# Performance work log

Hardware: AMD Instinct MI355X
Metric: run time of the kernel (lower is better)

## Reference

```python
import jax, jax.numpy as jnp
import numpy as np
import math

INPUT_SIZE = 768
OUTPUT_SIZE = 3072
INS = (8, 12, 8)     # inputs for size=768 (input_size < output_size, no swap)
OUTS = (16, 12, 16)  # outputs
# num singular values via quadratic formula from the torch code
_a = INS[2] * OUTS[2]
_b = INS[0] * OUTS[0] + INS[1] * OUTS[1]
_c = -INPUT_SIZE * OUTPUT_SIZE
NUM_S = int(((-_b + math.sqrt(_b * _b - 4 * _a * _c)) / (2 * _a)) // 1)  # = 134
N_TOKENS = 32768


def _xavier(key, shape, gain):
    # xavier_uniform over first-two-dims fan (matches torch fan computation:
    # fan_in = shape[1]*prod(shape[2:]), fan_out = shape[0]*prod(shape[2:]))
    recf = np.prod(shape[2:]).astype(np.float64) if len(shape) > 2 else 1.0
    fan_in = shape[1] * recf
    fan_out = shape[0] * recf
    bound = gain * math.sqrt(6.0 / (fan_in + fan_out))
    return jax.random.uniform(key, shape, jnp.float32, -bound, bound)


def setup_inputs() -> dict:
    key = jax.random.key(0)
    k0, k1, k2, k3 = jax.random.split(key, 4)
    g = math.sqrt(2.0)
    x = jax.random.normal(k0, (N_TOKENS, INPUT_SIZE), jnp.float32)
    W_1 = _xavier(k1, (INS[0], OUTS[0], NUM_S), g)            # (8,16,134)
    W_2 = _xavier(k2, (NUM_S, INS[1], OUTS[1], NUM_S), g)      # (134,12,12,134)
    W_3 = _xavier(k3, (NUM_S, INS[2], OUTS[2]), g)             # (134,8,16)
    b = jnp.zeros((OUTPUT_SIZE,), jnp.float32)
    return {"x": x, "W_1": W_1, "W_2": W_2, "W_3": W_3, "b": b}


def reference(x, W_1, W_2, W_3, b):
    # W[i,I,a, o,O,bb] = sum_{s,S} W_1[i,o,s] W_2[s,I,O,S] W_3[S,a,bb]
    W = jnp.einsum('ios,sIOS,Sab->iIaoOb', W_1, W_2, W_3)
    # rearrange '(i I a)(o O b)' -> row-major reshape
    W = W.reshape(INPUT_SIZE, OUTPUT_SIZE)
    return x @ W + b
```

## Files before the change

kernel.cpp:

```cpp
#include <hip/hip_runtime.h>


typedef unsigned short u16;
typedef unsigned int   u32;
typedef short s16x8 __attribute__((ext_vector_type(8)));
typedef float f32x4 __attribute__((ext_vector_type(4)));

__device__ __forceinline__ u16 f2bf(float f) {
  u32 u = __float_as_uint(f);
  u32 r = (u + 0x7FFFu + ((u >> 16) & 1u)) >> 16;
  return (u16)r;
}

__device__ __forceinline__ void gload_lds16(const void* g, void* l) {
  __builtin_amdgcn_global_load_lds(
      (const __attribute__((address_space(1))) void*)g,
      (__attribute__((address_space(3))) void*)l, 16, 0, 0);
}

__global__ __launch_bounds__(256) void xconv_kernel(const float* __restrict__ x,
                                                    u16* __restrict__ xb) {
  size_t idx = ((size_t)blockIdx.x * 256 + threadIdx.x) * 8;
  float4 v0 = *(const float4*)(x + idx);
  float4 v1 = *(const float4*)(x + idx + 4);
  uint4 o;
  o.x = (u32)f2bf(v0.x) | ((u32)f2bf(v0.y) << 16);
  o.y = (u32)f2bf(v0.z) | ((u32)f2bf(v0.w) << 16);
  o.z = (u32)f2bf(v1.x) | ((u32)f2bf(v1.y) << 16);
  o.w = (u32)f2bf(v1.z) | ((u32)f2bf(v1.w) << 16);
  *(uint4*)(xb + idx) = o;
}

__global__ __launch_bounds__(256) void a1_kernel(const float* __restrict__ W1,
                                                 const float* __restrict__ W2,
                                                 float* __restrict__ T1) {
  __shared__ float lW1[32 * 136];
  const int t = threadIdx.x;
  const int iog = blockIdx.y;
  const int ios = blockIdx.x * 256 + t;
  for (int idx = t; idx < 32 * 136; idx += 256) {
    int u = idx / 136, s = idx - u * 136;
    lW1[idx] = (s < 134) ? W1[(size_t)(iog * 32 + u) * 134 + s] : 0.f;
  }
  __syncthreads();
  const bool valid = ios < 19296;
  float acc[32];
#pragma unroll
  for (int u = 0; u < 32; u++) acc[u] = 0.f;
  for (int s4 = 0; s4 < 136; s4 += 4) {
    float wa = (valid && s4 + 0 < 134) ? W2[(size_t)(s4 + 0) * 19296 + ios] : 0.f;
    float wb = (valid && s4 + 1 < 134) ? W2[(size_t)(s4 + 1) * 19296 + ios] : 0.f;
    float wc = (valid && s4 + 2 < 134) ? W2[(size_t)(s4 + 2) * 19296 + ios] : 0.f;
    float wd = (valid && s4 + 3 < 134) ? W2[(size_t)(s4 + 3) * 19296 + ios] : 0.f;
#pragma unroll
    for (int u = 0; u < 32; u++) {
      float4 wv = *(const float4*)&lW1[u * 136 + s4];
      acc[u] += wv.x * wa + wv.y * wb + wv.z * wc + wv.w * wd;
    }
  }
  if (valid) {
#pragma unroll
    for (int u = 0; u < 32; u++)
      T1[(size_t)(iog * 32 + u) * 19296 + ios] = acc[u];
  }
}

__global__ __launch_bounds__(128) void a2_kernel(const float* __restrict__ T1,
                                                 const float* __restrict__ W3,
                                                 u16* __restrict__ Wt) {
  __shared__ float lT[12 * 136];
  __shared__ u16 lOut[192 * 8];
  const int t = threadIdx.x;
  const int io = blockIdx.x;
  const int I = blockIdx.y;
  const int i = io >> 4, o = io & 15;
  const float* src = T1 + (size_t)io * 19296 + (size_t)I * 1608;
  for (int idx = t; idx < 12 * 136; idx += 128) {
    int O = idx / 136, S = idx - O * 136;
    lT[idx] = (S < 134) ? src[O * 134 + S] : 0.f;
  }
  __syncthreads();
  float acc[12];
#pragma unroll
  for (int O = 0; O < 12; O++) acc[O] = 0.f;
  for (int S4 = 0; S4 < 136; S4 += 4) {
    float w0 = (S4 + 0 < 134) ? W3[(S4 + 0) * 128 + t] : 0.f;
    float w1 = (S4 + 1 < 134) ? W3[(S4 + 1) * 128 + t] : 0.f;
    float w2 = (S4 + 2 < 134) ? W3[(S4 + 2) * 128 + t] : 0.f;
    float w3 = (S4 + 3 < 134) ? W3[(S4 + 3) * 128 + t] : 0.f;
#pragma unroll
    for (int O = 0; O < 12; O++) {
      float4 tv = *(const float4*)&lT[O * 136 + S4];
      acc[O] += tv.x * w0 + tv.y * w1 + tv.z * w2 + tv.w * w3;
    }
  }
  const int a = t >> 4, b = t & 15;
#pragma unroll
  for (int O = 0; O < 12; O++) lOut[(O * 16 + b) * 8 + a] = f2bf(acc[O]);
  __syncthreads();
  for (int rr = t; rr < 192; rr += 128) {
    int col = o * 192 + rr;
    *(uint4*)&Wt[(size_t)col * 768 + i * 96 + I * 8] = *(const uint4*)&lOut[rr * 8];
  }
}


template <int N>
__device__ __forceinline__ void vmcnt_wait() {
  if constexpr (N == 12)     asm volatile("s_waitcnt vmcnt(12)" ::: "memory");
  else if constexpr (N == 8) asm volatile("s_waitcnt vmcnt(8)"  ::: "memory");
  else if constexpr (N == 4) asm volatile("s_waitcnt vmcnt(4)"  ::: "memory");
  else                       asm volatile("s_waitcnt vmcnt(0)"  ::: "memory");
}

__global__ __launch_bounds__(512, 2) void gemm_kernel(const u16* __restrict__ A,
                                                      const u16* __restrict__ Bt,
                                                      const float* __restrict__ bias,
                                                      float* __restrict__ C) {
  __shared__ u16 smem[4 * 16384];
  const int t = threadIdx.x;
  const int lane = t & 63, wid = t >> 6;
  const int wr = wid >> 2, wc = wid & 3;
  const int q = lane >> 4, l16 = lane & 15;

  const int bid = blockIdx.x;
  const int swz = (bid & 7) * 192 + (bid >> 3);
  const int nIdx = swz % 12, mIdx = swz / 12;
  const int blockM = mIdx * 256, blockN = nIdx * 256;

  const int kb_src = (((t & 3) ^ ((t >> 3) & 3)) << 4);
  const int rA = t >> 2;
  const u16* gAs = A  + (size_t)(blockM + rA) * 768 + (kb_src >> 1);
  const u16* gBs = Bt + (size_t)(blockN + rA) * 768 + (kb_src >> 1);

#define STAGE(b_, kt_) do {                                     \
    const u16* ga_ = gAs + (kt_) * 32;                          \
    const u16* gb_ = gBs + (kt_) * 32;                          \
    u16* lw_ = &smem[(b_) * 16384 + wid * 512];                 \
    gload_lds16(ga_,             lw_);                          \
    gload_lds16(ga_ + 128 * 768, lw_ + 4096);                   \
    gload_lds16(gb_,             lw_ + 8192);                   \
    gload_lds16(gb_ + 128 * 768, lw_ + 12288);                  \
  } while (0)

  f32x4 acc[8][4];
  const f32x4 z = {0.f, 0.f, 0.f, 0.f};
#pragma unroll
  for (int mi = 0; mi < 8; mi++)
#pragma unroll
    for (int ni = 0; ni < 4; ni++) acc[mi][ni] = z;

  const int koff = (q << 3) ^ (((l16 >> 1) & 3) << 3);
  const int aRow = wr * 128 + l16;
  const int bRow = wc * 64 + l16;

#define COMPUTE(bb_) do {                                                       \
    const u16* lA_ = &smem[(bb_) * 16384];                                      \
    const u16* lB_ = lA_ + 8192;                                                \
    s16x8 bg[4], af[4], af2[4];                                                 \
    _Pragma("unroll")                                                           \
    for (int ni = 0; ni < 4; ni++)                                              \
      bg[ni] = *(const s16x8*)&lB_[(bRow + ni * 16) * 32 + koff];               \
    _Pragma("unroll")                                                           \
    for (int mi = 0; mi < 4; mi++)                                              \
      af[mi] = *(const s16x8*)&lA_[(aRow + mi * 16) * 32 + koff];               \
    _Pragma("unroll")                                                           \
    for (int mi = 0; mi < 4; mi++)                                              \
      af2[mi] = *(const s16x8*)&lA_[(aRow + (mi + 4) * 16) * 32 + koff];        \
    __builtin_amdgcn_s_setprio(1);                                              \
    _Pragma("unroll")                                                           \
    for (int mi = 0; mi < 4; mi++)                                              \
      _Pragma("unroll")                                                         \
      for (int ni = 0; ni < 4; ni++)                                            \
        acc[mi][ni] = __builtin_amdgcn_mfma_f32_16x16x32_bf16(af[mi], bg[ni],   \
                                                              acc[mi][ni], 0, 0, 0); \
    __builtin_amdgcn_s_setprio(0);                                              \
    __builtin_amdgcn_s_setprio(1);                                              \
    _Pragma("unroll")                                                           \
    for (int mi = 0; mi < 4; mi++)                                              \
      _Pragma("unroll")                                                         \
      for (int ni = 0; ni < 4; ni++)                                            \
        acc[mi + 4][ni] = __builtin_amdgcn_mfma_f32_16x16x32_bf16(af2[mi], bg[ni], \
                                                              acc[mi + 4][ni], 0, 0, 0); \
    __builtin_amdgcn_s_setprio(0);                                              \
  } while (0)

  STAGE(0, 0);
  STAGE(1, 1);
  STAGE(2, 2);

  for (int tt = 0; tt < 21; ++tt) {
    STAGE((tt + 3) & 3, tt + 3);
    vmcnt_wait<12>();
    __builtin_amdgcn_s_barrier();
    __builtin_amdgcn_sched_barrier(0);
    COMPUTE(tt & 3);
    __builtin_amdgcn_sched_barrier(0);
    __builtin_amdgcn_s_barrier();
    __builtin_amdgcn_sched_barrier(0);
  }
  vmcnt_wait<8>();
  __builtin_amdgcn_s_barrier();
  __builtin_amdgcn_sched_barrier(0);
  COMPUTE(1);
  __builtin_amdgcn_sched_barrier(0);
  __builtin_amdgcn_s_barrier();
  vmcnt_wait<4>();
  __builtin_amdgcn_s_barrier();
  __builtin_amdgcn_sched_barrier(0);
  COMPUTE(2);
  __builtin_amdgcn_sched_barrier(0);
  __builtin_amdgcn_s_barrier();
  vmcnt_wait<0>();
  __builtin_amdgcn_s_barrier();
  __builtin_amdgcn_sched_barrier(0);
  COMPUTE(3);

  const int colBase = blockN + wc * 64 + l16;
#pragma unroll
  for (int ni = 0; ni < 4; ni++) {
    const int col = colBase + ni * 16;
    const float bv = bias[col];
#pragma unroll
    for (int mi = 0; mi < 8; mi++) {
      const int row = blockM + wr * 128 + mi * 16 + q * 4;
      float* cp = C + (size_t)row * 3072 + col;
      cp[0]        = acc[mi][ni][0] + bv;
      cp[3072]     = acc[mi][ni][1] + bv;
      cp[2 * 3072] = acc[mi][ni][2] + bv;
      cp[3 * 3072] = acc[mi][ni][3] + bv;
    }
  }
#undef STAGE
#undef COMPUTE
}

extern "C" void kernel_launch(void* const* d_in, const int* in_sizes, int n_in,
                              void* d_out, int out_size, void* d_ws, size_t ws_size,
                              hipStream_t stream) {
  const float* x  = (const float*)d_in[0];
  const float* W1 = (const float*)d_in[1];
  const float* W2 = (const float*)d_in[2];
  const float* W3 = (const float*)d_in[3];
  const float* b  = (const float*)d_in[4];
  float* out = (float*)d_out;

  char* ws = (char*)d_ws;
  u16* Xb   = (u16*)ws;
  u16* Wt   = (u16*)(ws + 50331648);
  float* T1 = (float*)(ws + 50331648 + 4718592);

  xconv_kernel<<<12288, 256, 0, stream>>>(x, Xb);
  a1_kernel<<<dim3(76, 4), 256, 0, stream>>>(W1, W2, T1);
  a2_kernel<<<dim3(128, 12), 128, 0, stream>>>(T1, W3, Wt);
  gemm_kernel<<<dim3(1536), 512, 0, stream>>>(Xb, Wt, b, out);
}
```

Measured before the change: 712.2 us.

## Interleave global-to-LDS prefetch with MFMA halves in GEMM main loop

Restructures the GEMM k-loop so that the prefetch of the A tile for k+3 is issued between the first LDS fragment reads and the first MFMA half, and the B tile prefetch between the second half's reads and its MFMAs. Each half is bracketed by extra barriers and lgkmcnt(0) waits, and the vmcnt gate moves to the end of each tile. The aim is to spread memory issue across the compute phase, ping-pong style, instead of issuing it all at the loop head. It adds more barriers per iteration and removes the sched_barrier hints, which could cost throughput.

```diff
diff --git a/kernel.cpp b/kernel.cpp
--- a/kernel.cpp
+++ b/kernel.cpp
@@ -107,11 +107,12 @@
 
 template <int N>
 __device__ __forceinline__ void vmcnt_wait() {
-  if constexpr (N == 12)     asm volatile("s_waitcnt vmcnt(12)" ::: "memory");
-  else if constexpr (N == 8) asm volatile("s_waitcnt vmcnt(8)"  ::: "memory");
+  if constexpr (N == 8)      asm volatile("s_waitcnt vmcnt(8)"  ::: "memory");
   else if constexpr (N == 4) asm volatile("s_waitcnt vmcnt(4)"  ::: "memory");
-  else                       asm volatile("s_waitcnt vmcnt(0)"  ::: "memory");
-}
+  else if constexpr (N == 0) asm volatile("s_waitcnt vmcnt(0)"  ::: "memory");
+}
+
+#define LGKMCNT0() asm volatile("s_waitcnt lgkmcnt(0)" ::: "memory")
 
 __global__ __launch_bounds__(512, 2) void gemm_kernel(const u16* __restrict__ A,
                                                       const u16* __restrict__ Bt,
@@ -133,16 +134,6 @@
   const u16* gAs = A  + (size_t)(blockM + rA) * 768 + (kb_src >> 1);
   const u16* gBs = Bt + (size_t)(blockN + rA) * 768 + (kb_src >> 1);
 
-#define STAGE(b_, kt_) do {                                     \
-    const u16* ga_ = gAs + (kt_) * 32;                          \
-    const u16* gb_ = gBs + (kt_) * 32;                          \
-    u16* lw_ = &smem[(b_) * 16384 + wid * 512];                 \
-    gload_lds16(ga_,             lw_);                          \
-    gload_lds16(ga_ + 128 * 768, lw_ + 4096);                   \
-    gload_lds16(gb_,             lw_ + 8192);                   \
-    gload_lds16(gb_ + 128 * 768, lw_ + 12288);                  \
-  } while (0)
-
   f32x4 acc[8][4];
   const f32x4 z = {0.f, 0.f, 0.f, 0.f};
 #pragma unroll
@@ -154,8 +145,8 @@
   const int aRow = wr * 128 + l16;
   const int bRow = wc * 64 + l16;
 
-#define COMPUTE(bb_) do {                                                       \
-    const u16* lA_ = &smem[(bb_) * 16384];                                      \
+#define TILE_BODY(kt_, STG_, GATE_) do {                                        \
+    const u16* lA_ = &smem[((kt_) & 3) * 16384];                                \
     const u16* lB_ = lA_ + 8192;                                                \
     s16x8 bg[4], af[4], af2[4];                                                 \
     _Pragma("unroll")                                                           \
@@ -164,9 +155,14 @@
     _Pragma("unroll")                                                           \
     for (int mi = 0; mi < 4; mi++)                                              \
       af[mi] = *(const s16x8*)&lA_[(aRow + mi * 16) * 32 + koff];               \
-    _Pragma("unroll")                                                           \
-    for (int mi = 0; mi < 4; mi++)                                              \
-      af2[mi] = *(const s16x8*)&lA_[(aRow + (mi + 4) * 16) * 32 + koff];        \
+    if (STG_) {                                                                 \
+      u16* lw_ = &smem[(((kt_) + 3) & 3) * 16384 + wid * 512];                  \
+      const u16* ga_ = gAs + ((kt_) + 3) * 32;                                  \
+      gload_lds16(ga_,             lw_);                                        \
+      gload_lds16(ga_ + 128 * 768, lw_ + 4096);                                 \
+    }                                                                           \
+    __builtin_amdgcn_s_barrier();                                               \
+    LGKMCNT0();                                                                 \
     __builtin_amdgcn_s_setprio(1);                                              \
     _Pragma("unroll")                                                           \
     for (int mi = 0; mi < 4; mi++)                                              \
@@ -175,6 +171,18 @@
         acc[mi][ni] = __builtin_amdgcn_mfma_f32_16x16x32_bf16(af[mi], bg[ni],   \
                                                               acc[mi][ni], 0, 0, 0); \
     __builtin_amdgcn_s_setprio(0);                                              \
+    __builtin_amdgcn_s_barrier();                                               \
+    _Pragma("unroll")                                                           \
+    for (int mi = 0; mi < 4; mi++)                                              \
+      af2[mi] = *(const s16x8*)&lA_[(aRow + (mi + 4) * 16) * 32 + koff];        \
+    if (STG_) {                                                                 \
+      u16* lw_ = &smem[(((kt_) + 3) & 3) * 16384 + wid * 512];                  \
+      const u16* gb_ = gBs + ((kt_) + 3) * 32;                                  \
+      gload_lds16(gb_,             lw_ + 8192);                                 \
+      gload_lds16(gb_ + 128 * 768, lw_ + 12288);                                \
+    }                                                                           \
+    __builtin_amdgcn_s_barrier();                                               \
+    LGKMCNT0();                                                                 \
     __builtin_amdgcn_s_setprio(1);                                              \
     _Pragma("unroll")                                                           \
     for (int mi = 0; mi < 4; mi++)                                              \
@@ -183,38 +191,31 @@
         acc[mi + 4][ni] = __builtin_amdgcn_mfma_f32_16x16x32_bf16(af2[mi], bg[ni], \
                                                               acc[mi + 4][ni], 0, 0, 0); \
     __builtin_amdgcn_s_setprio(0);                                              \
+    vmcnt_wait<GATE_>();                                                        \
+    __builtin_amdgcn_s_barrier();                                               \
   } while (0)
 
-  STAGE(0, 0);
-  STAGE(1, 1);
-  STAGE(2, 2);
-
-  for (int tt = 0; tt < 21; ++tt) {
-    STAGE((tt + 3) & 3, tt + 3);
-    vmcnt_wait<12>();
-    __builtin_amdgcn_s_barrier();
-    __builtin_amdgcn_sched_barrier(0);
-    COMPUTE(tt & 3);
-    __builtin_amdgcn_sched_barrier(0);
-    __builtin_amdgcn_s_barrier();
-    __builtin_amdgcn_sched_barrier(0);
+#pragma unroll
+  for (int pk = 0; pk < 3; ++pk) {
+    u16* lw_ = &smem[pk * 16384 + wid * 512];
+    const u16* ga_ = gAs + pk * 32;
+    const u16* gb_ = gBs + pk * 32;
+    gload_lds16(ga_,             lw_);
+    gload_lds16(ga_ + 128 * 768, lw_ + 4096);
+    gload_lds16(gb_,             lw_ + 8192);
+    gload_lds16(gb_ + 128 * 768, lw_ + 12288);
   }
   vmcnt_wait<8>();
   __builtin_amdgcn_s_barrier();
-  __builtin_amdgcn_sched_barrier(0);
-  COMPUTE(1);
-  __builtin_amdgcn_sched_barrier(0);
-  __builtin_amdgcn_s_barrier();
-  vmcnt_wait<4>();
-  __builtin_amdgcn_s_barrier();
-  __builtin_amdgcn_sched_barrier(0);
-  COMPUTE(2);
-  __builtin_amdgcn_sched_barrier(0);
-  __builtin_amdgcn_s_barrier();
-  vmcnt_wait<0>();
-  __builtin_amdgcn_s_barrier();
-  __builtin_amdgcn_sched_barrier(0);
-  COMPUTE(3);
+
+#pragma unroll 1
+  for (int kt = 0; kt < 21; ++kt) {
+    TILE_BODY(kt, 1, 8);
+  }
+  TILE_BODY(21, 0, 4);
+  TILE_BODY(22, 0, 0);
+  TILE_BODY(23, 0, -1);
+#undef TILE_BODY
 
   const int colBase = blockN + wc * 64 + l16;
 #pragma unroll
@@ -231,8 +232,6 @@
       cp[3 * 3072] = acc[mi][ni][3] + bv;
     }
   }
-#undef STAGE
-#undef COMPUTE
 }
 
 extern "C" void kernel_launch(void* const* d_in, const int* in_sizes, int n_in,
```

After: 704.4 us. No clear change (-1.1%).
